# Kernel tuning notes

Hardware: AMD Instinct MI355X
Metric: run time of the kernel (lower is better)

Reference implementation:

```python
import jax, jax.numpy as jnp
import numpy as np

EPS = 1e-5  # BatchNorm2d default eps


def _bn(x, gamma, beta, mean, var):
    # inference-mode BN over channel dim (NCHW)
    inv = gamma / jnp.sqrt(var + EPS)
    return x * inv[None, :, None, None] + (beta - mean * inv)[None, :, None, None]


def _shift(x):
    # 4 channel groups shifted by 1 pixel in 4 directions, zero-fill at borders
    C = x.shape[1]
    gc = C // 4
    g0, g1, g2, g3 = (x[:, i * gc:(i + 1) * gc] for i in range(4))
    g0 = jnp.pad(g0[:, :, :, :-1], ((0, 0), (0, 0), (0, 0), (1, 0)))  # shift right (W)
    g1 = jnp.pad(g1[:, :, 1:, :], ((0, 0), (0, 0), (0, 1), (0, 0)))   # shift up (H)
    g2 = jnp.pad(g2[:, :, :, 1:], ((0, 0), (0, 0), (0, 0), (0, 1)))   # shift left (W)
    g3 = jnp.pad(g3[:, :, :-1, :], ((0, 0), (0, 0), (1, 0), (0, 0)))  # shift down (H)
    return jnp.concatenate([g0, g1, g2, g3], axis=1)


def setup_inputs() -> dict:
    key = jax.random.key(0)
    ks = jax.random.split(key, 8)
    B, C1, C2, H, W = 16, 128, 256, 128, 128
    x = jax.random.normal(ks[0], (B, C1, H, W), dtype=jnp.float32)
    w_conv = jax.random.normal(ks[1], (C2, C1, 3, 3), dtype=jnp.float32) * (1.0 / np.sqrt(C1 * 9))
    w_1x1 = jax.random.normal(ks[2], (C2, C2, 1, 1), dtype=jnp.float32) * (1.0 / np.sqrt(C2))
    b_1x1 = jax.random.normal(ks[3], (C2,), dtype=jnp.float32) * 0.05
    gamma = jax.random.uniform(ks[4], (C2,), dtype=jnp.float32, minval=0.5, maxval=1.5)
    beta = jax.random.normal(ks[5], (C2,), dtype=jnp.float32) * 0.1
    bn_mean = jax.random.normal(ks[6], (C2,), dtype=jnp.float32) * 0.1
    bn_var = jax.random.uniform(ks[7], (C2,), dtype=jnp.float32, minval=0.5, maxval=1.5)
    return {"x": x, "w_conv": w_conv, "w_1x1": w_1x1, "b_1x1": b_1x1,
            "gamma": gamma, "beta": beta, "bn_mean": bn_mean, "bn_var": bn_var}


def reference(x, w_conv, w_1x1, b_1x1, gamma, beta, bn_mean, bn_var):
    # conv3x3 (stride 1, 'same' via autopad=1, no bias) + BN + SiLU
    y = jax.lax.conv_general_dilated(
        x, w_conv, window_strides=(1, 1), padding=((1, 1), (1, 1)),
        dimension_numbers=("NCHW", "OIHW", "NCHW"))
    y = jax.nn.silu(_bn(y, gamma, beta, bn_mean, bn_var))
    identity = y
    # shift + conv1x1 (with bias) + same BN + residual + SiLU
    z = _shift(y)
    z = jax.lax.conv_general_dilated(
        z, w_1x1, window_strides=(1, 1), padding=((0, 0), (0, 0)),
        dimension_numbers=("NCHW", "OIHW", "NCHW")) + b_1x1[None, :, None, None]
    z = _bn(z, gamma, beta, bn_mean, bn_var) + identity
    return jax.nn.silu(z)
```

## Files before the change

kernel.cpp:

```cpp
#include <hip/hip_runtime.h>

typedef unsigned short u16;
typedef unsigned int   u32;
typedef __bf16 bf16x8 __attribute__((ext_vector_type(8)));
typedef float  f32x4  __attribute__((ext_vector_type(4)));

__device__ __forceinline__ float bf2f(u16 v){ u32 u = ((u32)v) << 16; float f; __builtin_memcpy(&f,&u,4); return f; }
__device__ __forceinline__ u16 f2bf(float f){ u32 u; __builtin_memcpy(&u,&f,4); u32 r = (u + 0x7FFFu + ((u>>16)&1u)) >> 16; return (u16)r; }
__device__ __forceinline__ float silu(float v){ return v / (1.f + __expf(-v)); }

__device__ __forceinline__ void gload_lds16(const u16* g, u16* l){
  __builtin_amdgcn_global_load_lds((const __attribute__((address_space(1))) void*)g,
                                   (__attribute__((address_space(3))) void*)l, 16, 0, 0);
}

#define FENCE asm volatile("" ::: "memory")
#define BARRIER do{ FENCE; __builtin_amdgcn_s_barrier(); FENCE; }while(0)

#define HP 130
#define XPIX 128
#define YPIX 256
#define XIMG (HP*HP*XPIX)
#define YIMG (HP*HP*YPIX)

__global__ void prep_coef(const float* __restrict__ gamma, const float* __restrict__ beta,
                          const float* __restrict__ mean,  const float* __restrict__ var,
                          const float* __restrict__ b1, float2* __restrict__ coefA, float2* __restrict__ coefB){
  int c = threadIdx.x;
  float s = gamma[c] * rsqrtf(var[c] + 1e-5f);
  float t = beta[c] - mean[c] * s;
  coefA[c] = make_float2(s, t);
  coefB[c] = make_float2(s, b1[c] * s + t);
}

__global__ void repack_w3(const float* __restrict__ w, u16* __restrict__ w3p){
  int idx = blockIdx.x*256 + threadIdx.x;
  int n = idx / 1152, k = idx % 1152;
  int tap = k >> 7, c = k & 127;
  int kh = tap / 3, kw = tap % 3;
  w3p[idx] = f2bf(w[((n*128 + c)*3 + kh)*3 + kw]);
}

__global__ void repack_w1(const float* __restrict__ w, u16* __restrict__ w1p){
  int idx = blockIdx.x*256 + threadIdx.x;
  w1p[idx] = f2bf(w[idx]);
}

__device__ __forceinline__ void halo_pix(int pi, int& hp, int& wp){
  if (pi < 130){ hp = 0; wp = pi; }
  else if (pi < 260){ hp = 129; wp = pi - 130; }
  else { int j = pi - 260; hp = 1 + (j >> 1); wp = (j & 1) ? 129 : 0; }
}
__global__ void zero_halos(u16* __restrict__ xpad, u16* __restrict__ ypad, int cimg){
  int idx = blockIdx.x*256 + threadIdx.x;
  const int NX = cimg*516*16;
  uint4 z = make_uint4(0u,0u,0u,0u);
  if (idx < NX){
    int b = idx / (516*16), rr = idx % (516*16);
    int pi = rr >> 4, cch = rr & 15, hp, wp;
    halo_pix(pi, hp, wp);
    *(uint4*)(xpad + (((size_t)b*HP + hp)*HP + wp)*XPIX + cch*8) = z;
  } else {
    idx -= NX;
    if (idx < cimg*516*32){
      int b = idx / (516*32), rr = idx % (516*32);
      int pi = rr >> 5, cch = rr & 31, hp, wp;
      halo_pix(pi, hp, wp);
      *(uint4*)(ypad + (((size_t)b*HP + hp)*HP + wp)*YPIX + cch*8) = z;
    }
  }
}

__global__ __launch_bounds__(256) void transpose_x(const float* __restrict__ x, u16* __restrict__ xpad, int b0){
  __shared__ u16 s[64][66];
  const int tid = threadIdx.x, bid = blockIdx.x;
  const int ct = bid & 1, wt = (bid >> 1) & 1, row = bid >> 2;
  const int bl = row >> 7, h = row & 127;
  const int c0 = ct << 6, w0 = wt << 6;
  {
    const int lw = tid & 63, lc4 = tid >> 6;
    const size_t xb = ((size_t)(b0 + bl)*128)*16384 + (size_t)h*128 + w0 + lw;
    #pragma unroll
    for (int r = 0; r < 16; ++r){
      int c = r*4 + lc4;
      s[c][lw] = f2bf(x[xb + (size_t)(c0 + c)*16384]);
    }
  }
  __syncthreads();
  {
    const int lw = tid >> 5, lcp = (tid & 31) << 1;
    const size_t pb = ((size_t)bl*HP + h + 1)*HP;
    #pragma unroll
    for (int r = 0; r < 8; ++r){
      int w = r*8 + lw;
      u32 v = (u32)s[lcp][w] | ((u32)s[lcp+1][w] << 16);
      *(u32*)(xpad + (pb + (w0 + w + 1))*XPIX + c0 + lcp) = v;
    }
  }
}


__device__ __forceinline__ void stageA(u16* dst, const u16* ximg, int h0, int Ts, int ho, int t){
  const int tap = Ts >> 1, cc = (Ts & 1) << 6;
  const int kh = tap / 3, kw = tap - kh*3;
  const int lc = t & 7;
  #pragma unroll
  for (int q = 0; q < 2; ++q){
    const int r = ((t >> 6) << 4) + (q << 3) + ((t >> 3) & 7);
    const int p = (ho << 6) + r + (r & 64);
    const int hh = h0 + (p >> 7), ww = p & 127;
    const u16* src = ximg + (size_t)((hh + kh)*HP + ww + kw)*XPIX + cc + ((lc ^ (p & 7)) << 3);
    gload_lds16(src, dst + p*64 + lc*8);
  }
}

__device__ __forceinline__ void stageB3(u16* dst, const u16* w3p, int Ts, int bo, int t){
  const int lc = t & 7;
  #pragma unroll
  for (int q = 0; q < 2; ++q){
    const int r = ((t >> 6) << 4) + (q << 3) + ((t >> 3) & 7);
    const int n = ((r >> 5) << 6) + (bo << 5) + (r & 31);
    const u16* src = w3p + (size_t)n*1152 + Ts*64 + ((lc ^ (n & 7)) << 3);
    gload_lds16(src, dst + n*64 + lc*8);
  }
}

__device__ __forceinline__ bf16x8 ldfrag(const u16* s, int row, int c){
  return *(const bf16x8*)&s[row*64 + ((c ^ (row & 7)) << 3)];
}

__global__ __launch_bounds__(512, 2) void convA(const u16* __restrict__ xpad, const u16* __restrict__ w3p,
                                                const float2* __restrict__ coefA, u16* __restrict__ ypad){
  __shared__ u16 sA[2][256*64];
  __shared__ u16 sB[2][256*64];
  const int t = threadIdx.x;
  const int nwg = gridDim.x;
  const int bid = blockIdx.x;
  const int bsz = (bid & 7)*(nwg >> 3) + (bid >> 3);
  const int bl = bsz >> 6;
  const int h0 = (bsz & 63) << 1;
  const int lane = t & 63, wave = t >> 6;
  const int wm = wave & 1, wn = wave >> 1;
  const int quad = lane >> 4, l16 = lane & 15;
  const u16* ximg = xpad + (size_t)bl * XIMG;

  f32x4 acc[8][4];
  #pragma unroll
  for (int i = 0; i < 8; ++i)
    #pragma unroll
    for (int j = 0; j < 4; ++j){ f32x4 z = {0.f,0.f,0.f,0.f}; acc[i][j] = z; }

  stageA (sA[0], ximg, h0, 0, 0, t);
  stageB3(sB[0], w3p,      0, 0, t);
  stageB3(sB[0], w3p,      0, 1, t);
  stageA (sA[0], ximg, h0, 0, 1, t);
  asm volatile("s_waitcnt vmcnt(4)" ::: "memory");
  stageA (sA[1], ximg, h0, 1, 0, t);
  stageB3(sB[1], w3p,      1, 0, t);
  stageB3(sB[1], w3p,      1, 1, t);
  asm volatile("s_waitcnt vmcnt(6)" ::: "memory");
  BARRIER;

  for (int T = 0; T < 18; ++T){
    const int pr = T & 1;
    const u16* A = sA[pr];
    const u16* B = sB[pr];
    bf16x8 a[4][2], b0[2][2], b1[2][2];

    #pragma unroll
    for (int i = 0; i < 4; ++i){
      a[i][0] = ldfrag(A, wm*128 + i*16 + l16, quad);
      a[i][1] = ldfrag(A, wm*128 + i*16 + l16, 4 + quad);
    }
    #pragma unroll
    for (int j = 0; j < 2; ++j){
      b0[j][0] = ldfrag(B, wn*64 + j*16 + l16, quad);
      b0[j][1] = ldfrag(B, wn*64 + j*16 + l16, 4 + quad);
    }
    if (T + 1 < 18) stageA(sA[(T+1) & 1], ximg, h0, T+1, 1, t);
    BARRIER;
    __builtin_amdgcn_s_setprio(1);
    #pragma unroll
    for (int i = 0; i < 4; ++i)
      #pragma unroll
      for (int j = 0; j < 2; ++j){
        acc[i][j] = __builtin_amdgcn_mfma_f32_16x16x32_bf16(a[i][0], b0[j][0], acc[i][j], 0, 0, 0);
        acc[i][j] = __builtin_amdgcn_mfma_f32_16x16x32_bf16(a[i][1], b0[j][1], acc[i][j], 0, 0, 0);
      }
    __builtin_amdgcn_s_setprio(0);
    BARRIER;

    #pragma unroll
    for (int j = 0; j < 2; ++j){
      b1[j][0] = ldfrag(B, wn*64 + 32 + j*16 + l16, quad);
      b1[j][1] = ldfrag(B, wn*64 + 32 + j*16 + l16, 4 + quad);
    }
    if (T + 2 < 18) stageA(sA[pr], ximg, h0, T+2, 0, t);
    BARRIER;
    __builtin_amdgcn_s_setprio(1);
    #pragma unroll
    for (int i = 0; i < 4; ++i)
      #pragma unroll
      for (int j = 0; j < 2; ++j){
        acc[i][2+j] = __builtin_amdgcn_mfma_f32_16x16x32_bf16(a[i][0], b1[j][0], acc[i][2+j], 0, 0, 0);
        acc[i][2+j] = __builtin_amdgcn_mfma_f32_16x16x32_bf16(a[i][1], b1[j][1], acc[i][2+j], 0, 0, 0);
      }
    __builtin_amdgcn_s_setprio(0);
    BARRIER;

    #pragma unroll
    for (int i = 0; i < 4; ++i){
      a[i][0] = ldfrag(A, wm*128 + 64 + i*16 + l16, quad);
      a[i][1] = ldfrag(A, wm*128 + 64 + i*16 + l16, 4 + quad);
    }
    if (T + 2 < 18) stageB3(sB[pr], w3p, T+2, 0, t);
    BARRIER;
    __builtin_amdgcn_s_setprio(1);
    #pragma unroll
    for (int i = 0; i < 4; ++i)
      #pragma unroll
      for (int j = 0; j < 2; ++j){
        acc[4+i][2+j] = __builtin_amdgcn_mfma_f32_16x16x32_bf16(a[i][0], b1[j][0], acc[4+i][2+j], 0, 0, 0);
        acc[4+i][2+j] = __builtin_amdgcn_mfma_f32_16x16x32_bf16(a[i][1], b1[j][1], acc[4+i][2+j], 0, 0, 0);
      }
    __builtin_amdgcn_s_setprio(0);
    BARRIER;

    if (T + 2 < 18) stageB3(sB[pr], w3p, T+2, 1, t);
    BARRIER;
    __builtin_amdgcn_s_setprio(1);
    #pragma unroll
    for (int i = 0; i < 4; ++i)
      #pragma unroll
      for (int j = 0; j < 2; ++j){
        acc[4+i][j] = __builtin_amdgcn_mfma_f32_16x16x32_bf16(a[i][0], b0[j][0], acc[4+i][j], 0, 0, 0);
        acc[4+i][j] = __builtin_amdgcn_mfma_f32_16x16x32_bf16(a[i][1], b0[j][1], acc[4+i][j], 0, 0, 0);
      }
    __builtin_amdgcn_s_setprio(0);
    if (T < 16)       asm volatile("s_waitcnt vmcnt(6)" ::: "memory");
    else if (T == 16) asm volatile("s_waitcnt vmcnt(0)" ::: "memory");
    BARRIER;
  }

  float2 co[4];
  #pragma unroll
  for (int j = 0; j < 4; ++j) co[j] = coefA[wn*64 + j*16 + l16];
  #pragma unroll
  for (int ig = 0; ig < 8; ++ig){
    const int pb = wm*128 + ig*16 + quad*4;
    #pragma unroll
    for (int r = 0; r < 4; ++r){
      const int p = pb + r;
      const int hh = h0 + (p >> 7), ww = p & 127;
      u16* dst = ypad + ((size_t)(bl*HP + hh + 1)*HP + (ww + 1))*YPIX + wn*64;
      #pragma unroll
      for (int j = 0; j < 4; ++j){
        float v = acc[ig][j][r]*co[j].x + co[j].y;
        dst[j*16 + l16] = f2bf(silu(v));
      }
    }
  }
}

__global__ __launch_bounds__(256) void convB(const u16* __restrict__ ypad, const u16* __restrict__ w1p,
                                             const float2* __restrict__ coefB, float* __restrict__ out, int b0){
  __shared__ u16 sAct[4096];
  __shared__ u16 sW[4096];
  const int tid = threadIdx.x;
  const int nwg = gridDim.x;
  const int bidl = (blockIdx.x & 7)*(nwg >> 3) + (blockIdx.x >> 3);
  const int nt = bidl & 1, row = bidl >> 1;
  const int bl = row >> 7, h = row & 127;
  const int n0 = nt << 7;
  const int lane = tid & 63, wave = tid >> 6;
  const int wc = wave & 1, wpx = wave >> 1;
  const int quad = lane >> 4, l16 = lane & 15;
  const int r0 = tid >> 2, sub = tid & 3;

  f32x4 acc[4][4];
  #pragma unroll
  for (int i = 0; i < 4; ++i)
    #pragma unroll
    for (int j = 0; j < 4; ++j){ f32x4 zz = {0.f,0.f,0.f,0.f}; acc[i][j] = zz; }

  const size_t imgy = (size_t)bl * YIMG;
  const u16* w_row0 = w1p + (size_t)(n0 + r0)*256 + sub*8;
  const u16* w_row1 = w_row0 + (size_t)64*256;

  #pragma unroll
  for (int kt = 0; kt < 8; ++kt){
    const int g = kt >> 1;
    const int dhp = (g == 0 || g == 2) ? 1 : (g == 1 ? 2 : 0);
    const int dwp = (g == 1 || g == 3) ? 1 : (g == 0 ? 0 : 2);
    const size_t rb = imgy + (size_t)((h + dhp)*HP)*YPIX + kt*32 + sub*8;
    const u16* ga0 = ypad + rb + (size_t)(r0 + dwp)*YPIX;
    const u16* ga1 = ypad + rb + (size_t)(r0 + 64 + dwp)*YPIX;
    __syncthreads();
    gload_lds16(ga0, &sAct[tid*8]);
    gload_lds16(ga1, &sAct[2048 + tid*8]);
    gload_lds16(w_row0 + kt*32, &sW[tid*8]);
    gload_lds16(w_row1 + kt*32, &sW[2048 + tid*8]);
    __syncthreads();

    bf16x8 wf[4], af[4];
    #pragma unroll
    for (int i = 0; i < 4; ++i) wf[i] = *(const bf16x8*)&sW[(wc*64 + i*16 + l16)*32 + quad*8];
    #pragma unroll
    for (int j = 0; j < 4; ++j) af[j] = *(const bf16x8*)&sAct[(wpx*64 + j*16 + l16)*32 + quad*8];
    #pragma unroll
    for (int i = 0; i < 4; ++i)
      #pragma unroll
      for (int j = 0; j < 4; ++j)
        acc[i][j] = __builtin_amdgcn_mfma_f32_16x16x32_bf16(wf[i], af[j], acc[i][j], 0, 0, 0);
  }

  const size_t ybase = ((size_t)(bl*HP + h + 1))*HP*YPIX;
  const size_t obase = (size_t)(b0 + bl)*256*16384 + (size_t)h*128;
  #pragma unroll
  for (int i = 0; i < 4; ++i){
    const int chb = n0 + wc*64 + i*16 + quad*4;
    const float2 c0 = coefB[chb+0], c1 = coefB[chb+1], c2 = coefB[chb+2], c3 = coefB[chb+3];
    float* ob = out + obase + (size_t)chb*16384;
    #pragma unroll
    for (int j = 0; j < 4; ++j){
      const int p = wpx*64 + j*16 + l16;
      const ushort4 rv = *(const ushort4*)&ypad[ybase + (size_t)(p + 1)*YPIX + chb];
      ob[p]             = silu(acc[i][j][0]*c0.x + c0.y + bf2f(rv.x));
      ob[16384 + p]     = silu(acc[i][j][1]*c1.x + c1.y + bf2f(rv.y));
      ob[2*16384 + p]   = silu(acc[i][j][2]*c2.x + c2.y + bf2f(rv.z));
      ob[3*16384 + p]   = silu(acc[i][j][3]*c3.x + c3.y + bf2f(rv.w));
    }
  }
}

extern "C" void kernel_launch(void* const* d_in, const int* in_sizes, int n_in,
                              void* d_out, int out_size, void* d_ws, size_t ws_size,
                              hipStream_t stream){
  const float* x  = (const float*)d_in[0];
  const float* w3 = (const float*)d_in[1];
  const float* w1 = (const float*)d_in[2];
  const float* b1 = (const float*)d_in[3];
  const float* gm = (const float*)d_in[4];
  const float* bt = (const float*)d_in[5];
  const float* mn = (const float*)d_in[6];
  const float* vr = (const float*)d_in[7];
  float* outp = (float*)d_out;

  char* ws = (char*)d_ws;
  float2* coefA = (float2*)ws;
  float2* coefB = coefA + 256;
  u16*    w3p   = (u16*)(ws + 4096);
  u16*    w1p   = (u16*)(ws + 4096 + 589824);
  const size_t fixed = 4096 + 589824 + 131072;
  int cimg = 16;
  while (cimg > 1 && fixed + (size_t)cimg*12979200ull > ws_size) cimg >>= 1;
  u16* xpad = (u16*)(ws + fixed);
  u16* ypad = (u16*)(ws + fixed + (size_t)cimg*4326400ull);

  prep_coef<<<1, 256, 0, stream>>>(gm, bt, mn, vr, b1, coefA, coefB);
  repack_w3<<<1152, 256, 0, stream>>>(w3, w3p);
  repack_w1<<<256, 256, 0, stream>>>(w1, w1p);
  {
    int nthr = cimg*516*48;
    zero_halos<<<(nthr + 255)/256, 256, 0, stream>>>(xpad, ypad, cimg);
  }
  for (int b0 = 0; b0 < 16; b0 += cimg){
    transpose_x<<<4*128*cimg, 256, 0, stream>>>(x, xpad, b0);
    convA<<<64*cimg, 512, 0, stream>>>(xpad, w3p, coefA, ypad);
    convB<<<2*128*cimg, 256, 0, stream>>>(ypad, w1p, coefB, outp, b0);
  }
}
```

Before: 668.0 us.

## Precompute staging and fragment addresses in convA; double-buffer convB loads

In convA, the per-thread global and LDS staging addresses and the swizzled LDS fragment offsets are computed once before the main loop. Each stage then only adds a per-tap offset, which cuts integer address arithmetic inside the hot loop. In convB, the single-buffered LDS tiles become double-buffered so the next K-slice loads while MFMAs run on the current one, and setprio is raised around the MFMAs. The cost is more registers in convA for the precomputed addresses and twice the LDS in convB, which may lower occupancy.

```diff
diff --git a/kernel.cpp b/kernel.cpp
--- a/kernel.cpp
+++ b/kernel.cpp
@@ -100,33 +100,19 @@
 }
 
 
-__device__ __forceinline__ void stageA(u16* dst, const u16* ximg, int h0, int Ts, int ho, int t){
-  const int tap = Ts >> 1, cc = (Ts & 1) << 6;
-  const int kh = tap / 3, kw = tap - kh*3;
-  const int lc = t & 7;
-  #pragma unroll
-  for (int q = 0; q < 2; ++q){
-    const int r = ((t >> 6) << 4) + (q << 3) + ((t >> 3) & 7);
-    const int p = (ho << 6) + r + (r & 64);
-    const int hh = h0 + (p >> 7), ww = p & 127;
-    const u16* src = ximg + (size_t)((hh + kh)*HP + ww + kw)*XPIX + cc + ((lc ^ (p & 7)) << 3);
-    gload_lds16(src, dst + p*64 + lc*8);
-  }
-}
-
-__device__ __forceinline__ void stageB3(u16* dst, const u16* w3p, int Ts, int bo, int t){
-  const int lc = t & 7;
-  #pragma unroll
-  for (int q = 0; q < 2; ++q){
-    const int r = ((t >> 6) << 4) + (q << 3) + ((t >> 3) & 7);
-    const int n = ((r >> 5) << 6) + (bo << 5) + (r & 31);
-    const u16* src = w3p + (size_t)n*1152 + Ts*64 + ((lc ^ (n & 7)) << 3);
-    gload_lds16(src, dst + n*64 + lc*8);
-  }
-}
-
-__device__ __forceinline__ bf16x8 ldfrag(const u16* s, int row, int c){
-  return *(const bf16x8*)&s[row*64 + ((c ^ (row & 7)) << 3)];
+struct StgDesc { const u16* g[2][2]; int l[2][2]; };
+
+__device__ __forceinline__ int offA_of(int Ts){
+  int tap = Ts >> 1;
+  int kh = (tap*11) >> 5;
+  int kw = tap - kh*3;
+  return kh*(HP*XPIX) + kw*XPIX + ((Ts & 1) << 6);
+}
+
+template<int V>
+__device__ __forceinline__ void stage2(u16* lds, const StgDesc& d, int offE){
+  gload_lds16(d.g[V][0] + offE, lds + d.l[V][0]);
+  gload_lds16(d.g[V][1] + offE, lds + d.l[V][1]);
 }
 
 __global__ __launch_bounds__(512, 2) void convA(const u16* __restrict__ xpad, const u16* __restrict__ w3p,
@@ -142,42 +128,86 @@
   const int lane = t & 63, wave = t >> 6;
   const int wm = wave & 1, wn = wave >> 1;
   const int quad = lane >> 4, l16 = lane & 15;
+  const int lc = t & 7;
   const u16* ximg = xpad + (size_t)bl * XIMG;
 
+  StgDesc da, db;
+  #pragma unroll
+  for (int ho = 0; ho < 2; ++ho)
+    #pragma unroll
+    for (int q = 0; q < 2; ++q){
+      int r = ((t >> 6) << 4) + (q << 3) + ((t >> 3) & 7);
+      int p = (ho << 6) + r + (r & 64);
+      da.g[ho][q] = ximg + (size_t)((h0 + (p >> 7))*HP + (p & 127))*XPIX + ((lc ^ (p & 7)) << 3);
+      da.l[ho][q] = p*64 + lc*8;
+    }
+  #pragma unroll
+  for (int bo = 0; bo < 2; ++bo)
+    #pragma unroll
+    for (int q = 0; q < 2; ++q){
+      int r = ((t >> 6) << 4) + (q << 3) + ((t >> 3) & 7);
+      int n = ((r >> 5) << 6) + (bo << 5) + (r & 31);
+      db.g[bo][q] = w3p + (size_t)n*1152 + ((lc ^ (n & 7)) << 3);
+      db.l[bo][q] = n*64 + lc*8;
+    }
+
+  u32 fA[4][2][2], fB[2][2][2];
+  #pragma unroll
+  for (int i = 0; i < 4; ++i)
+    #pragma unroll
+    for (int hf = 0; hf < 2; ++hf)
+      #pragma unroll
+      for (int c = 0; c < 2; ++c){
+        int row = wm*128 + hf*64 + i*16 + l16;
+        fA[i][hf][c] = row*64 + (((c*4 + quad) ^ (row & 7)) << 3);
+      }
+  #pragma unroll
+  for (int j = 0; j < 2; ++j)
+    #pragma unroll
+    for (int hf = 0; hf < 2; ++hf)
+      #pragma unroll
+      for (int c = 0; c < 2; ++c){
+        int row = wn*64 + hf*32 + j*16 + l16;
+        fB[j][hf][c] = row*64 + (((c*4 + quad) ^ (row & 7)) << 3);
+      }
+
   f32x4 acc[8][4];
   #pragma unroll
   for (int i = 0; i < 8; ++i)
     #pragma unroll
     for (int j = 0; j < 4; ++j){ f32x4 z = {0.f,0.f,0.f,0.f}; acc[i][j] = z; }
 
-  stageA (sA[0], ximg, h0, 0, 0, t);
-  stageB3(sB[0], w3p,      0, 0, t);
-  stageB3(sB[0], w3p,      0, 1, t);
-  stageA (sA[0], ximg, h0, 0, 1, t);
-  asm volatile("s_waitcnt vmcnt(4)" ::: "memory");
-  stageA (sA[1], ximg, h0, 1, 0, t);
-  stageB3(sB[1], w3p,      1, 0, t);
-  stageB3(sB[1], w3p,      1, 1, t);
-  asm volatile("s_waitcnt vmcnt(6)" ::: "memory");
+  {
+    const int o0 = offA_of(0), o1 = offA_of(1);
+    stage2<0>(sA[0], da, o0);
+    stage2<0>(sB[0], db, 0);
+    stage2<1>(sB[0], db, 0);
+    stage2<1>(sA[0], da, o0);
+    stage2<0>(sA[1], da, o1);
+    stage2<0>(sB[1], db, 64);
+    stage2<1>(sB[1], db, 64);
+    asm volatile("s_waitcnt vmcnt(6)" ::: "memory");
+  }
   BARRIER;
 
   for (int T = 0; T < 18; ++T){
     const int pr = T & 1;
     const u16* A = sA[pr];
     const u16* B = sB[pr];
+    u16* An = sA[pr ^ 1];
     bf16x8 a[4][2], b0[2][2], b1[2][2];
 
     #pragma unroll
     for (int i = 0; i < 4; ++i){
-      a[i][0] = ldfrag(A, wm*128 + i*16 + l16, quad);
-      a[i][1] = ldfrag(A, wm*128 + i*16 + l16, 4 + quad);
+      a[i][0] = *(const bf16x8*)(A + fA[i][0][0]);
+      a[i][1] = *(const bf16x8*)(A + fA[i][0][1]);
     }
     #pragma unroll
     for (int j = 0; j < 2; ++j){
-      b0[j][0] = ldfrag(B, wn*64 + j*16 + l16, quad);
-      b0[j][1] = ldfrag(B, wn*64 + j*16 + l16, 4 + quad);
-    }
-    if (T + 1 < 18) stageA(sA[(T+1) & 1], ximg, h0, T+1, 1, t);
+      b0[j][0] = *(const bf16x8*)(B + fB[j][0][0]);
+      b0[j][1] = *(const bf16x8*)(B + fB[j][0][1]);
+    }
+    if (T + 1 < 18) stage2<1>(An, da, offA_of(T+1));
     BARRIER;
     __builtin_amdgcn_s_setprio(1);
     #pragma unroll
@@ -192,10 +222,10 @@
 
     #pragma unroll
     for (int j = 0; j < 2; ++j){
-      b1[j][0] = ldfrag(B, wn*64 + 32 + j*16 + l16, quad);
-      b1[j][1] = ldfrag(B, wn*64 + 32 + j*16 + l16, 4 + quad);
-    }
-    if (T + 2 < 18) stageA(sA[pr], ximg, h0, T+2, 0, t);
+      b1[j][0] = *(const bf16x8*)(B + fB[j][1][0]);
+      b1[j][1] = *(const bf16x8*)(B + fB[j][1][1]);
+    }
+    if (T + 2 < 18) stage2<0>((u16*)A, da, offA_of(T+2));
     BARRIER;
     __builtin_amdgcn_s_setprio(1);
     #pragma unroll
@@ -210,10 +240,10 @@
 
     #pragma unroll
     for (int i = 0; i < 4; ++i){
-      a[i][0] = ldfrag(A, wm*128 + 64 + i*16 + l16, quad);
-      a[i][1] = ldfrag(A, wm*128 + 64 + i*16 + l16, 4 + quad);
-    }
-    if (T + 2 < 18) stageB3(sB[pr], w3p, T+2, 0, t);
+      a[i][0] = *(const bf16x8*)(A + fA[i][1][0]);
+      a[i][1] = *(const bf16x8*)(A + fA[i][1][1]);
+    }
+    if (T + 2 < 18) stage2<0>((u16*)(B), db, (T+2)*64);
     BARRIER;
     __builtin_amdgcn_s_setprio(1);
     #pragma unroll
@@ -226,7 +256,7 @@
     __builtin_amdgcn_s_setprio(0);
     BARRIER;
 
-    if (T + 2 < 18) stageB3(sB[pr], w3p, T+2, 1, t);
+    if (T + 2 < 18) stage2<1>((u16*)(B), db, (T+2)*64);
     BARRIER;
     __builtin_amdgcn_s_setprio(1);
     #pragma unroll
@@ -262,10 +292,23 @@
   }
 }
 
+__device__ __forceinline__ void stgB(u16* act, u16* w, const u16* __restrict__ ypad,
+                                     size_t imgy, int h, int kt, int r0, int sub, int tid,
+                                     const u16* w_row0, const u16* w_row1){
+  const int g = kt >> 1;
+  const int dhp = (g == 0 || g == 2) ? 1 : (g == 1 ? 2 : 0);
+  const int dwp = (g == 1 || g == 3) ? 1 : (g == 0 ? 0 : 2);
+  const size_t rb = imgy + (size_t)((h + dhp)*HP)*YPIX + kt*32 + sub*8;
+  gload_lds16(ypad + rb + (size_t)(r0 + dwp)*YPIX,      act + tid*8);
+  gload_lds16(ypad + rb + (size_t)(r0 + 64 + dwp)*YPIX, act + 2048 + tid*8);
+  gload_lds16(w_row0 + kt*32, w + tid*8);
+  gload_lds16(w_row1 + kt*32, w + 2048 + tid*8);
+}
+
 __global__ __launch_bounds__(256) void convB(const u16* __restrict__ ypad, const u16* __restrict__ w1p,
                                              const float2* __restrict__ coefB, float* __restrict__ out, int b0){
-  __shared__ u16 sAct[4096];
-  __shared__ u16 sW[4096];
+  __shared__ u16 sAct[2][4096];
+  __shared__ u16 sW[2][4096];
   const int tid = threadIdx.x;
   const int nwg = gridDim.x;
   const int bidl = (blockIdx.x & 7)*(nwg >> 3) + (blockIdx.x >> 3);
@@ -287,31 +330,29 @@
   const u16* w_row0 = w1p + (size_t)(n0 + r0)*256 + sub*8;
   const u16* w_row1 = w_row0 + (size_t)64*256;
 
+  stgB(sAct[0], sW[0], ypad, imgy, h, 0, r0, sub, tid, w_row0, w_row1);
+  asm volatile("s_waitcnt vmcnt(0)" ::: "memory");
+  BARRIER;
+
   #pragma unroll
   for (int kt = 0; kt < 8; ++kt){
-    const int g = kt >> 1;
-    const int dhp = (g == 0 || g == 2) ? 1 : (g == 1 ? 2 : 0);
-    const int dwp = (g == 1 || g == 3) ? 1 : (g == 0 ? 0 : 2);
-    const size_t rb = imgy + (size_t)((h + dhp)*HP)*YPIX + kt*32 + sub*8;
-    const u16* ga0 = ypad + rb + (size_t)(r0 + dwp)*YPIX;
-    const u16* ga1 = ypad + rb + (size_t)(r0 + 64 + dwp)*YPIX;
-    __syncthreads();
-    gload_lds16(ga0, &sAct[tid*8]);
-    gload_lds16(ga1, &sAct[2048 + tid*8]);
-    gload_lds16(w_row0 + kt*32, &sW[tid*8]);
-    gload_lds16(w_row1 + kt*32, &sW[2048 + tid*8]);
-    __syncthreads();
+    const int cur = kt & 1;
+    if (kt < 7) stgB(sAct[cur^1], sW[cur^1], ypad, imgy, h, kt+1, r0, sub, tid, w_row0, w_row1);
 
     bf16x8 wf[4], af[4];
     #pragma unroll
-    for (int i = 0; i < 4; ++i) wf[i] = *(const bf16x8*)&sW[(wc*64 + i*16 + l16)*32 + quad*8];
-    #pragma unroll
-    for (int j = 0; j < 4; ++j) af[j] = *(const bf16x8*)&sAct[(wpx*64 + j*16 + l16)*32 + quad*8];
+    for (int i = 0; i < 4; ++i) wf[i] = *(const bf16x8*)&sW[cur][(wc*64 + i*16 + l16)*32 + quad*8];
+    #pragma unroll
+    for (int j = 0; j < 4; ++j) af[j] = *(const bf16x8*)&sAct[cur][(wpx*64 + j*16 + l16)*32 + quad*8];
+    __builtin_amdgcn_s_setprio(1);
     #pragma unroll
     for (int i = 0; i < 4; ++i)
       #pragma unroll
       for (int j = 0; j < 4; ++j)
         acc[i][j] = __builtin_amdgcn_mfma_f32_16x16x32_bf16(wf[i], af[j], acc[i][j], 0, 0, 0);
+    __builtin_amdgcn_s_setprio(0);
+    asm volatile("s_waitcnt vmcnt(0)" ::: "memory");
+    BARRIER;
   }
 
   const size_t ybase = ((size_t)(bl*HP + h + 1))*HP*YPIX;
```

New measurement: 668.5 us. About the same (+0.1%).
